# Performance work log

Hardware: AMD Instinct MI355X
Metric: run time of the kernel (lower is better)

Reference implementation:

```python
import jax, jax.numpy as jnp
import numpy as np

B, SQ, SK, H, NH = 8, 1024, 1024, 512, 4
D = H // NH
MASK_FILL = -2.0 ** 32 + 1
LN_EPS = 1e-5


def setup_inputs() -> dict:
    key = jax.random.key(0)
    ks = jax.random.split(key, 9)
    memory = jax.random.normal(ks[0], (B, SK, H), dtype=jnp.float32)
    decoder_input = jax.random.normal(ks[1], (B, SQ, H), dtype=jnp.float32)
    mask = jax.random.randint(ks[2], (B, SQ, SK), 0, 2).astype(bool)
    query_mask = jax.random.randint(ks[3], (B, SQ), 0, 2).astype(jnp.float32)
    # Linear weights stored torch-style as (out_dim, in_dim), xavier-ish scale
    scale = 1.0 / np.sqrt(H)
    Wk = jax.random.uniform(ks[4], (H, H), jnp.float32, -scale, scale)
    Wv = jax.random.uniform(ks[5], (H, H), jnp.float32, -scale, scale)
    Wq = jax.random.uniform(ks[6], (H, H), jnp.float32, -scale, scale)
    gamma = jnp.ones((H,), jnp.float32)
    beta = jnp.zeros((H,), jnp.float32)
    return {"memory": memory, "decoder_input": decoder_input, "mask": mask,
            "query_mask": query_mask, "Wk": Wk, "Wv": Wv, "Wq": Wq,
            "gamma": gamma, "beta": beta}


def reference(memory, decoder_input, mask, query_mask, Wk, Wv, Wq, gamma, beta):
    # projections (torch Linear: y = x @ W.T), split into heads
    k = jnp.einsum('bsh,oh->bso', memory, Wk).reshape(B, SK, NH, D)
    v = jnp.einsum('bsh,oh->bso', memory, Wv).reshape(B, SK, NH, D)
    q = jnp.einsum('bsh,oh->bso', decoder_input, Wq).reshape(B, SQ, NH, D)
    # scaled dot-product scores: [h, B, Sq, Sk]
    scores = jnp.einsum('bqhd,bkhd->hbqk', q, k) / jnp.sqrt(jnp.float32(D))
    scores = jnp.where(mask[None], jnp.float32(MASK_FILL), scores)
    attn = jax.nn.softmax(scores, axis=-1)
    # post-softmax multiplicative query mask
    attn = attn * query_mask[None, :, :, None]
    out = jnp.einsum('hbqk,bkhd->bqhd', attn, v).reshape(B, SQ, H)
    # residual + LayerNorm
    x = out + decoder_input
    mu = jnp.mean(x, axis=-1, keepdims=True)
    var = jnp.mean((x - mu) ** 2, axis=-1, keepdims=True)
    result = (x - mu) * jax.lax.rsqrt(var + LN_EPS) * gamma + beta
    # attn returned in torch layout [h*B, Sq, Sk]
    return result, attn.reshape(NH * B, SQ, SK)
```

## Files before the change

### kernel.cpp

```cpp
#include <hip/hip_runtime.h>
#include <hip/hip_bf16.h>
#include <stdint.h>

#define NB 8
#define NSQ 1024
#define NSK 1024
#define NHID 512
#define NHEAD 4
#define NDH 128

typedef __attribute__((ext_vector_type(8))) short short8;
typedef __attribute__((ext_vector_type(4))) float f32x4;

__device__ __forceinline__ unsigned short f2b(float f) {
  unsigned int u = __builtin_bit_cast(unsigned int, f);
  u = u + 0x7FFFu + ((u >> 16) & 1u);
  return (unsigned short)(u >> 16);
}

__device__ __forceinline__ short8 pack8(float4 a, float4 b) {
  short8 o;
  o[0] = (short)f2b(a.x); o[1] = (short)f2b(a.y);
  o[2] = (short)f2b(a.z); o[3] = (short)f2b(a.w);
  o[4] = (short)f2b(b.x); o[5] = (short)f2b(b.y);
  o[6] = (short)f2b(b.z); o[7] = (short)f2b(b.w);
  return o;
}

__device__ __forceinline__ void gl2lds16(const unsigned short* g, unsigned short* l) {
  __builtin_amdgcn_global_load_lds(
      (const __attribute__((address_space(1))) void*)g,
      (__attribute__((address_space(3))) void*)l, 16, 0, 0);
}

__global__ __launch_bounds__(256) void cvt_blocked(
    const float* __restrict__ dec, const float* __restrict__ mem,
    const float* __restrict__ Wq, const float* __restrict__ Wk,
    const float* __restrict__ Wv, unsigned short* __restrict__ decB,
    unsigned short* __restrict__ memB, unsigned short* __restrict__ WB) {
  const int bid = blockIdx.x, tid = threadIdx.x;
  const float* src;
  unsigned short* dst;
  int base_row;
  if (bid < 2048) { src = dec; dst = decB; base_row = bid * 4; }
  else if (bid < 4096) { src = mem; dst = memB; base_row = (bid - 2048) * 4; }
  else {
    int w = bid - 4096;
    int wi = w >> 7;
    src = (wi == 0) ? Wq : (wi == 1) ? Wk : Wv;
    dst = WB + (size_t)wi * 262144;
    base_row = (w & 127) * 4;
  }
  const int row = base_row + (tid >> 6);
  const int kpos = (tid & 63) * 8;
  const float* s = src + (size_t)row * 512 + kpos;
  float4 a0 = *(const float4*)s;
  float4 a1 = *(const float4*)(s + 4);
  const int mt = row >> 7, kt = kpos >> 6, pr = row & 127, c = (kpos & 63) >> 3;
  *(short8*)&dst[(size_t)(mt * 8 + kt) * 8192 + pr * 64 + ((c ^ (pr & 7)) * 8)] =
      pack8(a0, a1);
}

__global__ void pack_mask(const int* __restrict__ m, unsigned int* __restrict__ mw) {
  int w = blockIdx.x * blockDim.x + threadIdx.x;
  const int* src = m + (size_t)w * 32;
  unsigned int bits = 0;
#pragma unroll
  for (int j = 0; j < 32; j += 4) {
    int4 v = *(const int4*)(src + j);
    bits |= (v.x ? 1u << j : 0u) | (v.y ? 1u << (j + 1) : 0u) |
            (v.z ? 1u << (j + 2) : 0u) | (v.w ? 1u << (j + 3) : 0u);
  }
  int row = w >> 5, wi = w & 31;
  mw[(size_t)row * 32 + ((wi & 3) * 8 + (wi >> 2))] = bits;
}

__global__ __launch_bounds__(256) void proj_gemm_all(
    const unsigned short* __restrict__ decB, const unsigned short* __restrict__ memB,
    const unsigned short* __restrict__ WB, unsigned short* __restrict__ Cb) {
  __shared__ unsigned short tA[2][8192];
  __shared__ unsigned short tB[2][8192];
  const int z = blockIdx.z;
  const unsigned short* A = (z == 0) ? decB : memB;
  const unsigned short* W = WB + (size_t)z * 262144;
  unsigned short* C = Cb + (size_t)z * 4194304;
  const bool tr = (z == 2);
  const int tid = threadIdx.x, lane = tid & 63, wave = tid >> 6;
  const int mt = blockIdx.x, h = blockIdx.y;
  const int wm = (wave & 1) * 64, wn = (wave >> 1) * 64;
  const int r15 = lane & 15, hi = lane >> 4;

  auto stage = [&](int kt, int sel) {
#pragma unroll
    for (int i = 0; i < 4; ++i) {
      int ci = i * 4 + wave;
      gl2lds16(A + (size_t)(mt * 8 + kt) * 8192 + ci * 512 + lane * 8,
               &tA[sel][ci * 512 + lane * 8]);
      gl2lds16(W + (size_t)(h * 8 + kt) * 8192 + ci * 512 + lane * 8,
               &tB[sel][ci * 512 + lane * 8]);
    }
  };

  f32x4 acc[4][4];
  for (int i = 0; i < 4; ++i)
    for (int j = 0; j < 4; ++j) acc[i][j] = (f32x4){0.f, 0.f, 0.f, 0.f};

  stage(0, 0);
  __syncthreads();
  for (int kt = 0; kt < 8; ++kt) {
    const int sel = kt & 1;
    if (kt < 7) stage(kt + 1, sel ^ 1);
    __builtin_amdgcn_s_setprio(1);
#pragma unroll
    for (int kk = 0; kk < 2; ++kk) {
      short8 af[4], bf[4];
#pragma unroll
      for (int mi = 0; mi < 4; ++mi) {
        int row = wm + mi * 16 + r15;
        af[mi] = *(short8*)&tA[sel][row * 64 + (((kk * 4 + hi) ^ (row & 7)) * 8)];
      }
#pragma unroll
      for (int ni = 0; ni < 4; ++ni) {
        int row = wn + ni * 16 + r15;
        bf[ni] = *(short8*)&tB[sel][row * 64 + (((kk * 4 + hi) ^ (row & 7)) * 8)];
      }
#pragma unroll
      for (int mi = 0; mi < 4; ++mi)
#pragma unroll
        for (int ni = 0; ni < 4; ++ni)
          acc[mi][ni] = __builtin_amdgcn_mfma_f32_16x16x32_bf16(
              af[mi], bf[ni], acc[mi][ni], 0, 0, 0);
    }
    __builtin_amdgcn_s_setprio(0);
    __syncthreads();
  }

#pragma unroll
  for (int mi = 0; mi < 4; ++mi)
#pragma unroll
    for (int ni = 0; ni < 4; ++ni)
#pragma unroll
      for (int r = 0; r < 4; ++r) {
        int m = mt * 128 + wm + mi * 16 + hi * 4 + r;
        int d = wn + ni * 16 + r15;
        int bq = m >> 10, q = m & 1023, t = q >> 7, pr = q & 127;
        size_t pbase = (size_t)((bq * 4 + h) * 8 + t) * 16384;
        unsigned short v = f2b(acc[mi][ni][r]);
        if (!tr)
          C[pbase + pr * 128 + (((d >> 3) ^ (pr & 7)) * 8) + (d & 7)] = v;
        else
          C[pbase + d * 128 + (((pr >> 3) ^ (d & 7)) * 8) + (pr & 7)] = v;
      }
}

__global__ __launch_bounds__(512, 4) void attn_s_kernel(
    const unsigned short* __restrict__ Qb, const unsigned short* __restrict__ Kb,
    const unsigned int* __restrict__ maskp, const float* __restrict__ qmask,
    float* __restrict__ attn) {
  __shared__ unsigned short tQ[32 * 128];
  __shared__ unsigned short buf0[128 * 128];
  __shared__ unsigned short buf1[128 * 128];
  __shared__ float redsum[32][8];
  const int L = blockIdx.x;
  const int r_ = L & 7;
  const int j_ = L >> 3;
  const int qt = j_ & 31;
  const int hb = (j_ >> 5) * 8 + r_;
  const int h = hb >> 3, b = hb & 7;
  const int q0 = qt * 32;
  const int tid = threadIdx.x;
  const int lane = tid & 63, wave = tid >> 6;
  const int r15 = lane & 15, hi = lane >> 4;

  auto stageK = [&](int t, unsigned short* buf) {
    const unsigned short* p = Kb + (size_t)((b * 4 + h) * 8 + t) * 16384;
#pragma unroll
    for (int i = 0; i < 4; ++i) {
      int ci = i * 8 + wave;
      gl2lds16(p + ci * 512 + lane * 8, buf + ci * 512 + lane * 8);
    }
  };
  {
    const unsigned short* p =
        Qb + (size_t)((b * 4 + h) * 8 + (q0 >> 7)) * 16384 + (q0 & 127) * 128;
    gl2lds16(p + wave * 512 + lane * 8, tQ + wave * 512 + lane * 8);
  }
  stageK(0, buf0);
  __syncthreads();

  f32x4 acc[2][8];
#pragma unroll
  for (int g = 0; g < 2; ++g)
#pragma unroll
    for (int t = 0; t < 8; ++t) acc[g][t] = (f32x4){0.f, 0.f, 0.f, 0.f};

#pragma unroll
  for (int t = 0; t < 8; ++t) {
    if (t < 7) stageK(t + 1, (t & 1) ? buf0 : buf1);
    const unsigned short* kb = (t & 1) ? buf1 : buf0;
    __builtin_amdgcn_s_setprio(1);
#pragma unroll
    for (int ks = 0; ks < 4; ++ks) {
      const int sw = ((ks * 4 + hi) ^ (r15 & 7)) * 8;
      short8 bk = *(const short8*)&kb[(wave * 16 + r15) * 128 + sw];
#pragma unroll
      for (int g = 0; g < 2; ++g) {
        short8 aqv = *(const short8*)&tQ[(g * 16 + r15) * 128 + sw];
        acc[g][t] = __builtin_amdgcn_mfma_f32_16x16x32_bf16(aqv, bk, acc[g][t], 0, 0, 0);
      }
    }
    __builtin_amdgcn_s_setprio(0);
    __syncthreads();
  }

  const float isd = 0.08838834764831845f;
  const int sh = (wave & 1) * 16 + r15;
#pragma unroll
  for (int g = 0; g < 2; ++g)
#pragma unroll
    for (int r = 0; r < 4; ++r) {
      const unsigned int* mrow =
          maskp + ((size_t)(b * NSQ) + q0 + g * 16 + hi * 4 + r) * 32 + (wave >> 1) * 8;
      uint4 wa = *(const uint4*)mrow;
      uint4 wb = *(const uint4*)(mrow + 4);
      unsigned int mw8[8] = {wa.x, wa.y, wa.z, wa.w, wb.x, wb.y, wb.z, wb.w};
      float sm = 0.f;
#pragma unroll
      for (int t = 0; t < 8; ++t) {
        unsigned int bit = (mw8[t] >> sh) & 1u;
        float s = acc[g][t][r] * isd;
        float e = __expf(bit ? -4294967296.0f : s);
        acc[g][t][r] = e;
        sm += e;
      }
      sm += __shfl_xor(sm, 1);
      sm += __shfl_xor(sm, 2);
      sm += __shfl_xor(sm, 4);
      sm += __shfl_xor(sm, 8);
      if (r15 == 0) redsum[g * 16 + hi * 4 + r][wave] = sm;
    }
  __syncthreads();
#pragma unroll
  for (int g = 0; g < 2; ++g)
#pragma unroll
    for (int r = 0; r < 4; ++r) {
      float4 a = *(float4*)&redsum[g * 16 + hi * 4 + r][0];
      float4 c = *(float4*)&redsum[g * 16 + hi * 4 + r][4];
      float sum = (a.x + a.y + a.z + a.w) + (c.x + c.y + c.z + c.w);
      float scl = qmask[b * NSQ + q0 + g * 16 + hi * 4 + r] / sum;
#pragma unroll
      for (int t = 0; t < 8; ++t) acc[g][t][r] *= scl;
    }

#pragma unroll
  for (int g = 0; g < 2; ++g) {
    float* abase =
        attn + ((size_t)hb * NSQ + q0 + g * 16 + hi * 4) * NSK + wave * 16 + r15;
#pragma unroll
    for (int t = 0; t < 8; ++t)
#pragma unroll
      for (int r = 0; r < 4; ++r) abase[(r << 10) + t * 128] = acc[g][t][r];
  }
}

__global__ __launch_bounds__(256) void pv_gemm(const float* __restrict__ attn,
                                               const unsigned short* __restrict__ Vtb,
                                               float* __restrict__ outh) {
  __shared__ unsigned short tA[64 * 128];
  __shared__ unsigned short tB[128 * 128];
  const int L = blockIdx.x;
  const int r_ = L & 7, q_ = (L >> 3) & 15, s_ = L >> 7;
  const int hb = s_ * 8 + r_;
  const int h = hb >> 3, b = hb & 7;
  const int m0 = q_ * 64;
  const int tid = threadIdx.x;
  const int lane = tid & 63;
  const int wave = tid >> 6;
  const int wn = wave * 32;
  const int r15 = lane & 15, hi = lane >> 4;
  const float* Abase = attn + (size_t)hb * NSQ * NSK;

  f32x4 acc[4][2];
  for (int i = 0; i < 4; ++i)
    for (int j = 0; j < 2; ++j) acc[i][j] = (f32x4){0.f, 0.f, 0.f, 0.f};

  for (int kt = 0; kt < 8; ++kt) {
    {
      const unsigned short* p = Vtb + (size_t)((b * 4 + h) * 8 + kt) * 16384;
#pragma unroll
      for (int i = 0; i < 8; ++i) {
        int ci = i * 4 + wave;
        gl2lds16(p + ci * 512 + lane * 8, tB + ci * 512 + lane * 8);
      }
    }
#pragma unroll
    for (int it = 0; it < 4; ++it) {
      int idx = it * 256 + tid;
      int row = idx >> 4, c = idx & 15;
      const float* sa = Abase + (size_t)(m0 + row) * NSK + kt * 128 + c * 8;
      float4 a0 = *(const float4*)sa;
      float4 a1 = *(const float4*)(sa + 4);
      *(short8*)&tA[row * 128 + ((c ^ (row & 7)) * 8)] = pack8(a0, a1);
    }
    __syncthreads();
    __builtin_amdgcn_s_setprio(1);
#pragma unroll
    for (int ks = 0; ks < 4; ++ks) {
      short8 af[4], bf[2];
#pragma unroll
      for (int mi = 0; mi < 4; ++mi) {
        int row = mi * 16 + r15;
        af[mi] = *(short8*)&tA[row * 128 + (((ks * 4 + hi) ^ (row & 7)) * 8)];
      }
#pragma unroll
      for (int ni = 0; ni < 2; ++ni) {
        int row = wn + ni * 16 + r15;
        bf[ni] = *(short8*)&tB[row * 128 + (((ks * 4 + hi) ^ (row & 7)) * 8)];
      }
#pragma unroll
      for (int mi = 0; mi < 4; ++mi)
#pragma unroll
        for (int ni = 0; ni < 2; ++ni)
          acc[mi][ni] = __builtin_amdgcn_mfma_f32_16x16x32_bf16(
              af[mi], bf[ni], acc[mi][ni], 0, 0, 0);
    }
    __builtin_amdgcn_s_setprio(0);
    __syncthreads();
  }
#pragma unroll
  for (int mi = 0; mi < 4; ++mi)
#pragma unroll
    for (int ni = 0; ni < 2; ++ni)
#pragma unroll
      for (int r = 0; r < 4; ++r) {
        int m = m0 + mi * 16 + hi * 4 + r;
        int n = wn + ni * 16 + r15;
        outh[(size_t)(b * NSQ + m) * NHID + h * NDH + n] = acc[mi][ni][r];
      }
}

__global__ __launch_bounds__(256) void ln_kernel(const float* __restrict__ outh,
                                                 const float* __restrict__ dec,
                                                 const float* __restrict__ gamma,
                                                 const float* __restrict__ beta,
                                                 float* __restrict__ result) {
  const int tid = threadIdx.x;
  const int lane = tid & 63, wave = tid >> 6;
  const size_t row = (size_t)blockIdx.x * 4 + wave;
  const float* xr = outh + row * NHID;
  const float* dr = dec + row * NHID;
  float v[8];
  float s = 0.f;
  for (int j = 0; j < 2; ++j) {
    float4 a = *(const float4*)(xr + lane * 8 + j * 4);
    float4 d = *(const float4*)(dr + lane * 8 + j * 4);
    v[j * 4 + 0] = a.x + d.x; v[j * 4 + 1] = a.y + d.y;
    v[j * 4 + 2] = a.z + d.z; v[j * 4 + 3] = a.w + d.w;
  }
  for (int j = 0; j < 8; ++j) s += v[j];
  for (int off = 32; off > 0; off >>= 1) s += __shfl_xor(s, off);
  float mu = s * (1.f / 512.f);
  float s2 = 0.f;
  for (int j = 0; j < 8; ++j) {
    float d = v[j] - mu;
    s2 += d * d;
  }
  for (int off = 32; off > 0; off >>= 1) s2 += __shfl_xor(s2, off);
  float rstd = rsqrtf(s2 * (1.f / 512.f) + 1e-5f);
  float* out = result + row * NHID;
  for (int j = 0; j < 2; ++j) {
    float4 g = *(const float4*)(gamma + lane * 8 + j * 4);
    float4 bt = *(const float4*)(beta + lane * 8 + j * 4);
    float4 o;
    o.x = (v[j * 4 + 0] - mu) * rstd * g.x + bt.x;
    o.y = (v[j * 4 + 1] - mu) * rstd * g.y + bt.y;
    o.z = (v[j * 4 + 2] - mu) * rstd * g.z + bt.z;
    o.w = (v[j * 4 + 3] - mu) * rstd * g.w + bt.w;
    *(float4*)(out + lane * 8 + j * 4) = o;
  }
}

extern "C" void kernel_launch(void* const* d_in, const int* in_sizes, int n_in,
                              void* d_out, int out_size, void* d_ws, size_t ws_size,
                              hipStream_t stream) {
  const float* memory = (const float*)d_in[0];
  const float* dec = (const float*)d_in[1];
  const int* mask = (const int*)d_in[2];
  const float* qmask = (const float*)d_in[3];
  const float* Wk = (const float*)d_in[4];
  const float* Wv = (const float*)d_in[5];
  const float* Wq = (const float*)d_in[6];
  const float* gamma = (const float*)d_in[7];
  const float* beta = (const float*)d_in[8];

  char* ws = (char*)d_ws;
  unsigned short* decBb = (unsigned short*)(ws + 0);
  unsigned short* memBb = (unsigned short*)(ws + 8388608);
  float* outh = (float*)(ws + 0);
  unsigned short* WB = (unsigned short*)(ws + 16777216);
  unsigned short* QKVb = (unsigned short*)(ws + 18350080);
  unsigned int* maskw = (unsigned int*)(ws + 43515904);

  unsigned short* Qb = QKVb;
  unsigned short* Kb = QKVb + 4194304;
  unsigned short* Vtb = QKVb + 8388608;

  float* resultp = (float*)d_out;
  float* attnp = resultp + 4194304;

  cvt_blocked<<<dim3(4480), dim3(256), 0, stream>>>(dec, memory, Wq, Wk, Wv, decBb,
                                                    memBb, WB);
  pack_mask<<<dim3(1024), dim3(256), 0, stream>>>(mask, maskw);
  proj_gemm_all<<<dim3(64, 4, 3), dim3(256), 0, stream>>>(decBb, memBb, WB, QKVb);

  attn_s_kernel<<<dim3(1024), dim3(512), 0, stream>>>(Qb, Kb, maskw, qmask, attnp);
  pv_gemm<<<dim3(512), dim3(256), 0, stream>>>(attnp, Vtb, outh);
  ln_kernel<<<dim3(2048), dim3(256), 0, stream>>>(outh, dec, gamma, beta, resultp);
}
```

Before: 117.7 us.

## Merge mask packing into conversion kernel, remap projection grid, use nontemporal and bf16 intermediates

Merges the mask bit-packing kernel into the fp32-to-bf16 conversion kernel, saving one launch. Flattens the projection GEMM grid to 1D with a remapped block order, likely to spread work across XCDs. Adds nontemporal loads and stores on the large streaming attention buffers, and stores the PV output as bf16 so the LayerNorm kernel reads half the bytes. The bf16 intermediate adds rounding error before the residual and LayerNorm.

```diff
diff --git a/kernel.cpp b/kernel.cpp
--- a/kernel.cpp
+++ b/kernel.cpp
@@ -11,6 +11,7 @@
 
 typedef __attribute__((ext_vector_type(8))) short short8;
 typedef __attribute__((ext_vector_type(4))) float f32x4;
+typedef __attribute__((ext_vector_type(4))) int i32x4;
 
 __device__ __forceinline__ unsigned short f2b(float f) {
   unsigned int u = __builtin_bit_cast(unsigned int, f);
@@ -18,7 +19,12 @@
   return (unsigned short)(u >> 16);
 }
 
-__device__ __forceinline__ short8 pack8(float4 a, float4 b) {
+__device__ __forceinline__ float b2f(unsigned short s) {
+  unsigned int u = ((unsigned int)s) << 16;
+  return __builtin_bit_cast(float, u);
+}
+
+__device__ __forceinline__ short8 pack8v(f32x4 a, f32x4 b) {
   short8 o;
   o[0] = (short)f2b(a.x); o[1] = (short)f2b(a.y);
   o[2] = (short)f2b(a.z); o[3] = (short)f2b(a.w);
@@ -33,12 +39,27 @@
       (__attribute__((address_space(3))) void*)l, 16, 0, 0);
 }
 
-__global__ __launch_bounds__(256) void cvt_blocked(
+__global__ __launch_bounds__(256) void cvt_pack(
     const float* __restrict__ dec, const float* __restrict__ mem,
     const float* __restrict__ Wq, const float* __restrict__ Wk,
-    const float* __restrict__ Wv, unsigned short* __restrict__ decB,
-    unsigned short* __restrict__ memB, unsigned short* __restrict__ WB) {
+    const float* __restrict__ Wv, const int* __restrict__ mask,
+    unsigned short* __restrict__ decB, unsigned short* __restrict__ memB,
+    unsigned short* __restrict__ WB, unsigned int* __restrict__ mw) {
   const int bid = blockIdx.x, tid = threadIdx.x;
+  if (bid >= 4480) {
+    int w = (bid - 4480) * 256 + tid;
+    const int* src = mask + (size_t)w * 32;
+    unsigned int bits = 0;
+#pragma unroll
+    for (int j = 0; j < 32; j += 4) {
+      i32x4 v = __builtin_nontemporal_load((const i32x4*)(src + j));
+      bits |= (v.x ? 1u << j : 0u) | (v.y ? 1u << (j + 1) : 0u) |
+              (v.z ? 1u << (j + 2) : 0u) | (v.w ? 1u << (j + 3) : 0u);
+    }
+    int row = w >> 5, wi = w & 31;
+    mw[(size_t)row * 32 + ((wi & 3) * 8 + (wi >> 2))] = bits;
+    return;
+  }
   const float* src;
   unsigned short* dst;
   int base_row;
@@ -54,25 +75,11 @@
   const int row = base_row + (tid >> 6);
   const int kpos = (tid & 63) * 8;
   const float* s = src + (size_t)row * 512 + kpos;
-  float4 a0 = *(const float4*)s;
-  float4 a1 = *(const float4*)(s + 4);
+  f32x4 a0 = __builtin_nontemporal_load((const f32x4*)s);
+  f32x4 a1 = __builtin_nontemporal_load((const f32x4*)(s + 4));
   const int mt = row >> 7, kt = kpos >> 6, pr = row & 127, c = (kpos & 63) >> 3;
   *(short8*)&dst[(size_t)(mt * 8 + kt) * 8192 + pr * 64 + ((c ^ (pr & 7)) * 8)] =
-      pack8(a0, a1);
-}
-
-__global__ void pack_mask(const int* __restrict__ m, unsigned int* __restrict__ mw) {
-  int w = blockIdx.x * blockDim.x + threadIdx.x;
-  const int* src = m + (size_t)w * 32;
-  unsigned int bits = 0;
-#pragma unroll
-  for (int j = 0; j < 32; j += 4) {
-    int4 v = *(const int4*)(src + j);
-    bits |= (v.x ? 1u << j : 0u) | (v.y ? 1u << (j + 1) : 0u) |
-            (v.z ? 1u << (j + 2) : 0u) | (v.w ? 1u << (j + 3) : 0u);
-  }
-  int row = w >> 5, wi = w & 31;
-  mw[(size_t)row * 32 + ((wi & 3) * 8 + (wi >> 2))] = bits;
+      pack8v(a0, a1);
 }
 
 __global__ __launch_bounds__(256) void proj_gemm_all(
@@ -80,13 +87,16 @@
     const unsigned short* __restrict__ WB, unsigned short* __restrict__ Cb) {
   __shared__ unsigned short tA[2][8192];
   __shared__ unsigned short tB[2][8192];
-  const int z = blockIdx.z;
+  const int bid = blockIdx.x;
+  const int w = (bid & 7) * 96 + (bid >> 3);
+  const int z = w >> 8;
+  const int rem = w & 255;
+  const int mt = rem >> 2, h = rem & 3;
   const unsigned short* A = (z == 0) ? decB : memB;
   const unsigned short* W = WB + (size_t)z * 262144;
   unsigned short* C = Cb + (size_t)z * 4194304;
   const bool tr = (z == 2);
   const int tid = threadIdx.x, lane = tid & 63, wave = tid >> 6;
-  const int mt = blockIdx.x, h = blockIdx.y;
   const int wm = (wave & 1) * 64, wn = (wave >> 1) * 64;
   const int r15 = lane & 15, hi = lane >> 4;
 
@@ -259,13 +269,14 @@
 #pragma unroll
     for (int t = 0; t < 8; ++t)
 #pragma unroll
-      for (int r = 0; r < 4; ++r) abase[(r << 10) + t * 128] = acc[g][t][r];
+      for (int r = 0; r < 4; ++r)
+        __builtin_nontemporal_store(acc[g][t][r], abase + (r << 10) + t * 128);
   }
 }
 
 __global__ __launch_bounds__(256) void pv_gemm(const float* __restrict__ attn,
                                                const unsigned short* __restrict__ Vtb,
-                                               float* __restrict__ outh) {
+                                               unsigned short* __restrict__ outh) {
   __shared__ unsigned short tA[64 * 128];
   __shared__ unsigned short tB[128 * 128];
   const int L = blockIdx.x;
@@ -298,9 +309,9 @@
       int idx = it * 256 + tid;
       int row = idx >> 4, c = idx & 15;
       const float* sa = Abase + (size_t)(m0 + row) * NSK + kt * 128 + c * 8;
-      float4 a0 = *(const float4*)sa;
-      float4 a1 = *(const float4*)(sa + 4);
-      *(short8*)&tA[row * 128 + ((c ^ (row & 7)) * 8)] = pack8(a0, a1);
+      f32x4 a0 = __builtin_nontemporal_load((const f32x4*)sa);
+      f32x4 a1 = __builtin_nontemporal_load((const f32x4*)(sa + 4));
+      *(short8*)&tA[row * 128 + ((c ^ (row & 7)) * 8)] = pack8v(a0, a1);
     }
     __syncthreads();
     __builtin_amdgcn_s_setprio(1);
@@ -335,11 +346,11 @@
       for (int r = 0; r < 4; ++r) {
         int m = m0 + mi * 16 + hi * 4 + r;
         int n = wn + ni * 16 + r15;
-        outh[(size_t)(b * NSQ + m) * NHID + h * NDH + n] = acc[mi][ni][r];
-      }
-}
-
-__global__ __launch_bounds__(256) void ln_kernel(const float* __restrict__ outh,
+        outh[(size_t)(b * NSQ + m) * NHID + h * NDH + n] = f2b(acc[mi][ni][r]);
+      }
+}
+
+__global__ __launch_bounds__(256) void ln_kernel(const unsigned short* __restrict__ outh,
                                                  const float* __restrict__ dec,
                                                  const float* __restrict__ gamma,
                                                  const float* __restrict__ beta,
@@ -347,15 +358,17 @@
   const int tid = threadIdx.x;
   const int lane = tid & 63, wave = tid >> 6;
   const size_t row = (size_t)blockIdx.x * 4 + wave;
-  const float* xr = outh + row * NHID;
+  const unsigned short* xr = outh + row * NHID;
   const float* dr = dec + row * NHID;
   float v[8];
   float s = 0.f;
+  short8 xv = *(const short8*)(xr + lane * 8);
   for (int j = 0; j < 2; ++j) {
-    float4 a = *(const float4*)(xr + lane * 8 + j * 4);
     float4 d = *(const float4*)(dr + lane * 8 + j * 4);
-    v[j * 4 + 0] = a.x + d.x; v[j * 4 + 1] = a.y + d.y;
-    v[j * 4 + 2] = a.z + d.z; v[j * 4 + 3] = a.w + d.w;
+    v[j * 4 + 0] = b2f((unsigned short)xv[j * 4 + 0]) + d.x;
+    v[j * 4 + 1] = b2f((unsigned short)xv[j * 4 + 1]) + d.y;
+    v[j * 4 + 2] = b2f((unsigned short)xv[j * 4 + 2]) + d.z;
+    v[j * 4 + 3] = b2f((unsigned short)xv[j * 4 + 3]) + d.w;
   }
   for (int j = 0; j < 8; ++j) s += v[j];
   for (int off = 32; off > 0; off >>= 1) s += __shfl_xor(s, off);
@@ -396,7 +409,7 @@
   char* ws = (char*)d_ws;
   unsigned short* decBb = (unsigned short*)(ws + 0);
   unsigned short* memBb = (unsigned short*)(ws + 8388608);
-  float* outh = (float*)(ws + 0);
+  unsigned short* outh = (unsigned short*)(ws + 0);
   unsigned short* WB = (unsigned short*)(ws + 16777216);
   unsigned short* QKVb = (unsigned short*)(ws + 18350080);
   unsigned int* maskw = (unsigned int*)(ws + 43515904);
@@ -408,10 +421,9 @@
   float* resultp = (float*)d_out;
   float* attnp = resultp + 4194304;
 
-  cvt_blocked<<<dim3(4480), dim3(256), 0, stream>>>(dec, memory, Wq, Wk, Wv, decBb,
-                                                    memBb, WB);
-  pack_mask<<<dim3(1024), dim3(256), 0, stream>>>(mask, maskw);
-  proj_gemm_all<<<dim3(64, 4, 3), dim3(256), 0, stream>>>(decBb, memBb, WB, QKVb);
+  cvt_pack<<<dim3(5504), dim3(256), 0, stream>>>(dec, memory, Wq, Wk, Wv, mask,
+                                                 decBb, memBb, WB, maskw);
+  proj_gemm_all<<<dim3(768), dim3(256), 0, stream>>>(decBb, memBb, WB, QKVb);
 
   attn_s_kernel<<<dim3(1024), dim3(512), 0, stream>>>(Qb, Kb, maskw, qmask, attnp);
   pv_gemm<<<dim3(512), dim3(256), 0, stream>>>(attnp, Vtb, outh);
```

Result: slower. 160.0 us (+36.0%).
